# Performance work log

Measured on AMD Instinct MI355X. Metric: run time of the kernel, lower is better.

Reference implementation:

```python
import jax, jax.numpy as jnp
import numpy as np
from jax import lax

IMAGE_SIZE = 1280
STRIDE = 32
FMP = IMAGE_SIZE // STRIDE          # 40
BPC = 5                             # boxes per cell (5 anchors)
NUM_CLASSES = 80
NMS_THRESH = 0.5
CONF_THRESH = 0.3
N_BOX = FMP * FMP * BPC             # 8000 candidates
ANCHOR_SIZE = np.array([[17, 25], [55, 75], [92, 206], [202, 21], [289, 311]], dtype=np.float32)


def _make_anchors():
    # generate_anchors: per-cell (x,y) grid repeated for each of BPC anchors, tiled anchor wh
    ys, xs = jnp.meshgrid(jnp.arange(FMP, dtype=jnp.float32), jnp.arange(FMP, dtype=jnp.float32), indexing='ij')
    xy = jnp.stack([xs, ys], axis=-1).reshape(-1, 1, 2)                       # [HW,1,2]
    anchor_xy = jnp.broadcast_to(xy, (FMP * FMP, BPC, 2)).reshape(-1, 2)      # [N,2]
    anchor_wh = jnp.broadcast_to(jnp.asarray(ANCHOR_SIZE)[None], (FMP * FMP, BPC, 2)).reshape(-1, 2)
    return jnp.concatenate([anchor_xy, anchor_wh], axis=-1)                   # [N,4]


def setup_inputs() -> dict:
    key = jax.random.key(0)
    k = jax.random.split(key, 5)
    return {
        'cls_feat': jax.random.normal(k[0], (1, 512, FMP, FMP), jnp.float32),
        'reg_feat': jax.random.normal(k[1], (1, 512, FMP, FMP), jnp.float32),
        'w_obj': jax.random.normal(k[2], (BPC, 512), jnp.float32) * 0.02,
        'b_obj': jnp.zeros((BPC,), jnp.float32),
        'w_cls': jax.random.normal(k[3], (NUM_CLASSES * BPC, 512), jnp.float32) * 0.02,
        'b_cls': jnp.zeros((NUM_CLASSES * BPC,), jnp.float32),
        'w_reg': jax.random.normal(k[4], (4 * BPC, 512), jnp.float32) * 0.02,
        'b_reg': jnp.zeros((4 * BPC,), jnp.float32),
    }


def reference(cls_feat, reg_feat, w_obj, b_obj, w_cls, b_cls, w_reg, b_reg):
    # 1x1 convs as channel contractions, already permuted to NHWC like permute(0,2,3,1)
    obj = (jnp.einsum('bchw,oc->bhwo', reg_feat, w_obj) + b_obj).reshape(-1, 1)            # [N,1]
    cls = (jnp.einsum('bchw,oc->bhwo', cls_feat, w_cls) + b_cls).reshape(-1, NUM_CLASSES)  # [N,C]
    reg = (jnp.einsum('bchw,oc->bhwo', reg_feat, w_reg) + b_reg).reshape(-1, 4)            # [N,4]

    scores = jnp.sqrt(jax.nn.sigmoid(obj) * jax.nn.sigmoid(cls))                           # [N,C]

    # decode_boxes
    anchors = _make_anchors()
    ctr = (jax.nn.sigmoid(reg[:, :2]) + anchors[:, :2]) * STRIDE
    wh = jnp.exp(reg[:, 2:]) * anchors[:, 2:]
    bboxes = jnp.concatenate([ctr - wh * 0.5, ctr + wh * 0.5], axis=-1)                    # [N,4] x1y1x2y2

    # postprocess: per-box best class + confidence filter
    labels = jnp.argmax(scores, axis=1)
    score = jnp.take_along_axis(scores, labels[:, None], axis=1)[:, 0]
    valid = score >= CONF_THRESH

    # faithful to original nms(): it re-interprets decoded x1y1x2y2 as cxcywh before IoU
    b2 = jnp.concatenate([bboxes[:, :2] - bboxes[:, 2:] * 0.5,
                          bboxes[:, :2] + bboxes[:, 2:] * 0.5], axis=-1)

    # greedy per-class NMS == global greedy with cross-class IoU gated to 0
    order = jnp.argsort(-score)
    bs = b2[order]
    ls = labels[order]
    vs = valid[order]
    areas = (bs[:, 2] - bs[:, 0]) * (bs[:, 3] - bs[:, 1])
    xx1 = jnp.maximum(bs[:, None, 0], bs[None, :, 0])
    yy1 = jnp.maximum(bs[:, None, 1], bs[None, :, 1])
    xx2 = jnp.minimum(bs[:, None, 2], bs[None, :, 2])
    yy2 = jnp.minimum(bs[:, None, 3], bs[None, :, 3])
    inter = jnp.maximum(1e-10, xx2 - xx1) * jnp.maximum(1e-10, yy2 - yy1)
    iou = inter / (areas[:, None] + areas[None, :] - inter + 1e-14)                        # [N,N]
    same = ls[:, None] == ls[None, :]

    idx = jnp.arange(N_BOX)

    def body(k, supp):
        active = vs[k] & jnp.logical_not(supp[k])
        row = active & (iou[k] > NMS_THRESH) & same[k] & (idx > k)
        return supp | row

    supp = lax.fori_loop(0, N_BOX, body, jnp.zeros(N_BOX, bool))
    keep = jnp.zeros(N_BOX, bool).at[order].set(vs & jnp.logical_not(supp))

    # fixed-size masked outputs (original returns variable-length filtered arrays)
    return bboxes, score, labels, keep
```

## Files before the change

### kernel.cpp

```cpp
#include <hip/hip_runtime.h>
#include <math.h>

#define FMPX 40
#define NPOS 1600
#define NCLS 80
#define NBOX 8000
#define KDIM 512
#define CAP  256

__constant__ float c_aw[5] = {17.f, 55.f, 92.f, 202.f, 289.f};
__constant__ float c_ah[5] = {25.f, 75.f, 206.f, 21.f, 311.f};

__device__ __forceinline__ float sigf(float x) { return 1.0f / (1.0f + expf(-x)); }
__device__ __forceinline__ float rlanef(float v, int lane) {
    return __uint_as_float(__builtin_amdgcn_readlane(__float_as_uint(v), lane));
}

__global__ __launch_bounds__(64) void k_gemm(
    const float* __restrict__ cls_feat, const float* __restrict__ reg_feat,
    const float* __restrict__ w_obj, const float* __restrict__ b_obj,
    const float* __restrict__ w_cls, const float* __restrict__ b_cls,
    const float* __restrict__ w_reg, const float* __restrict__ b_reg,
    float* __restrict__ clsRaw,
    float* __restrict__ roRaw)
{
    __shared__ float Ws[4 * KDIM];
    const int mTile = blockIdx.x;
    const int nTile = blockIdx.y;
    const int hw0   = mTile * 128;
    const bool isCls = (nTile < 100);
    const float* feat = isCls ? cls_feat : reg_feat;
    const int lane = threadIdx.x;
    const int oBase = isCls ? nTile * 4 : (nTile - 100) * 4;

    for (int i = lane * 4; i < 4 * KDIM; i += 64 * 4) {
        int r = i >> 9, k = i & 511;
        const float* src;
        bool valid = true;
        if (isCls) {
            src = w_cls + (oBase + r) * KDIM + k;
        } else {
            int o = oBase + r;
            if (o < 5)       src = w_obj + o * KDIM + k;
            else if (o < 25) src = w_reg + (o - 5) * KDIM + k;
            else           { src = w_obj; valid = false; }
        }
        float4 v = valid ? *(const float4*)src : make_float4(0.f, 0.f, 0.f, 0.f);
        *(float4*)&Ws[i] = v;
    }

    float bias[4];
    bool ok[4];
#pragma unroll
    for (int j = 0; j < 4; j++) {
        int o = oBase + j;
        if (isCls)      { bias[j] = b_cls[o];     ok[j] = true; }
        else if (o < 5) { bias[j] = b_obj[o];     ok[j] = true; }
        else if (o < 25){ bias[j] = b_reg[o - 5]; ok[j] = true; }
        else            { bias[j] = 0.0f;         ok[j] = false; }
    }

    const bool ok1 = (hw0 + 64 + lane) < NPOS;
    const float* apa = feat + hw0 + lane;
    const float* apb = feat + (ok1 ? hw0 + 64 + lane : hw0 + lane);

    float A0a[8], A0b[8], A1a[8], A1b[8];
#pragma unroll
    for (int t = 0; t < 8; t++) { A0a[t] = apa[t * NPOS];       A0b[t] = apb[t * NPOS]; }
#pragma unroll
    for (int t = 0; t < 8; t++) { A1a[t] = apa[(8 + t) * NPOS]; A1b[t] = apb[(8 + t) * NPOS]; }

    __syncthreads();

    float acc[4], acd[4];
#pragma unroll
    for (int j = 0; j < 4; j++) { acc[j] = 0.f; acd[j] = 0.f; }

    for (int kk = 0; kk < KDIM - 16; kk += 16) {
#pragma unroll
        for (int j = 0; j < 4; j++) {
            const float* wp = &Ws[j * KDIM + kk];
#pragma unroll
            for (int t = 0; t < 8; t++) {
                acc[j] += A0a[t] * wp[t];
                acd[j] += A0b[t] * wp[t];
            }
        }
#pragma unroll
        for (int t = 0; t < 8; t++) { A0a[t] = apa[(kk + 16 + t) * NPOS]; A0b[t] = apb[(kk + 16 + t) * NPOS]; }
#pragma unroll
        for (int j = 0; j < 4; j++) {
            const float* wp = &Ws[j * KDIM + kk + 8];
#pragma unroll
            for (int t = 0; t < 8; t++) {
                acc[j] += A1a[t] * wp[t];
                acd[j] += A1b[t] * wp[t];
            }
        }
#pragma unroll
        for (int t = 0; t < 8; t++) { A1a[t] = apa[(kk + 24 + t) * NPOS]; A1b[t] = apb[(kk + 24 + t) * NPOS]; }
    }
    {
        const int kk = KDIM - 16;
#pragma unroll
        for (int j = 0; j < 4; j++) {
            const float* wp = &Ws[j * KDIM + kk];
#pragma unroll
            for (int t = 0; t < 8; t++) {
                acc[j] += A0a[t] * wp[t];
                acd[j] += A0b[t] * wp[t];
            }
        }
#pragma unroll
        for (int j = 0; j < 4; j++) {
            const float* wp = &Ws[j * KDIM + kk + 8];
#pragma unroll
            for (int t = 0; t < 8; t++) {
                acc[j] += A1a[t] * wp[t];
                acd[j] += A1b[t] * wp[t];
            }
        }
    }

    const int hw  = hw0 + lane;
    const int hw2 = hw + 64;
    if (isCls) {
        float4 r0 = make_float4(acc[0] + bias[0], acc[1] + bias[1],
                                acc[2] + bias[2], acc[3] + bias[3]);
        *(float4*)&clsRaw[hw * 400 + oBase] = r0;
        if (ok1) {
            float4 r1 = make_float4(acd[0] + bias[0], acd[1] + bias[1],
                                    acd[2] + bias[2], acd[3] + bias[3]);
            *(float4*)&clsRaw[hw2 * 400 + oBase] = r1;
        }
    } else {
#pragma unroll
        for (int j = 0; j < 4; j++) {
            int o = oBase + j;
            if (ok[j]) {
                roRaw[hw * 25 + o] = acc[j] + bias[j];
                if (ok1) roRaw[hw2 * 25 + o] = acd[j] + bias[j];
            }
        }
    }
}

__global__ __launch_bounds__(256) void k_box(
    const float* __restrict__ clsRaw, const float* __restrict__ roRaw,
    float* __restrict__ out,
    float4* __restrict__ nmsBox, float* __restrict__ nmsArea,
    float2* __restrict__ sl)
{
    const int n = blockIdx.x * 4 + (threadIdx.x >> 6);
    const int lane = threadIdx.x & 63;
    const int hw = n / 5, a = n % 5;

    const float sobj = sigf(roRaw[hw * 25 + a]);
    const float* cbase = clsRaw + hw * 400 + a * 80;

    const int l4 = (lane < 20) ? lane : 19;
    float4 cs = *(const float4*)(cbase + l4 * 4);

    float s0 = sqrtf(sobj * sigf(cs.x));
    float s1 = sqrtf(sobj * sigf(cs.y));
    float s2 = sqrtf(sobj * sigf(cs.z));
    float s3 = sqrtf(sobj * sigf(cs.w));
    float v = s0; int bi = l4 * 4;
    if (s1 > v) { v = s1; bi = l4 * 4 + 1; }
    if (s2 > v) { v = s2; bi = l4 * 4 + 2; }
    if (s3 > v) { v = s3; bi = l4 * 4 + 3; }
    if (lane >= 20) { v = -1.0f; bi = 0x7FFFFFFF; }

#pragma unroll
    for (int off = 32; off >= 1; off >>= 1) {
        float ov = __shfl_xor(v, off);
        int   oi = __shfl_xor(bi, off);
        if (ov > v || (ov == v && oi < bi)) { v = ov; bi = oi; }
    }

    if (lane == 0) {
        const float* rp = roRaw + hw * 25 + 5 + a * 4;
        float r0 = rp[0], r1 = rp[1], r2 = rp[2], r3 = rp[3];
        float gx = (float)(hw % FMPX), gy = (float)(hw / FMPX);
        float cx = (sigf(r0) + gx) * 32.0f;
        float cy = (sigf(r1) + gy) * 32.0f;
        float wv = expf(r2) * c_aw[a];
        float hv = expf(r3) * c_ah[a];
        float x1 = cx - wv * 0.5f, y1 = cy - hv * 0.5f;
        float x2 = cx + wv * 0.5f, y2 = cy + hv * 0.5f;

        out[n * 4 + 0] = x1; out[n * 4 + 1] = y1;
        out[n * 4 + 2] = x2; out[n * 4 + 3] = y2;
        out[32000 + n] = v;
        out[40000 + n] = (float)bi;
        out[48000 + n] = 0.0f;
        sl[n] = make_float2(v, (float)bi);

        float nx1 = x1 - x2 * 0.5f, ny1 = y1 - y2 * 0.5f;
        float nx2 = x1 + x2 * 0.5f, ny2 = y1 + y2 * 0.5f;
        nmsBox[n]  = make_float4(nx1, ny1, nx2, ny2);
        nmsArea[n] = (nx2 - nx1) * (ny2 - ny1);
    }
}

__global__ __launch_bounds__(64) void k_nms(
    const float2* __restrict__ sl,
    const float4* __restrict__ nmsBox, const float* __restrict__ nmsArea,
    float* __restrict__ keepOut)
{
    const int c = blockIdx.x;
    const int lane = threadIdx.x;

    __shared__ float ss[CAP];
    __shared__ int   si[CAP];
    __shared__ int   cnt;

    if (lane == 0) cnt = 0;
    __syncthreads();

    const float4* sl4 = (const float4*)sl;
    for (int base = 0; base < NBOX / 2; base += 512) {
        float4 buf[8];
#pragma unroll
        for (int b = 0; b < 8; b++) {
            int q = base + b * 64 + lane;
            buf[b] = (q < NBOX / 2) ? sl4[q] : make_float4(0.f, 0.f, 0.f, 0.f);
        }
#pragma unroll
        for (int b = 0; b < 8; b++) {
            int q = base + b * 64 + lane;
            if (q < NBOX / 2) {
                if (buf[b].x >= 0.3f && (int)buf[b].y == c) {
                    int t = atomicAdd(&cnt, 1);
                    if (t < CAP) { ss[t] = buf[b].x; si[t] = 2 * q; }
                }
                if (buf[b].z >= 0.3f && (int)buf[b].w == c) {
                    int t = atomicAdd(&cnt, 1);
                    if (t < CAP) { ss[t] = buf[b].z; si[t] = 2 * q + 1; }
                }
            }
        }
    }
    __syncthreads();

    int m = cnt;
    if (m > CAP) m = CAP;

    int P = 2;
    while (P < m) P <<= 1;
    for (int i = lane; i < P; i += 64) {
        if (i >= m) { ss[i] = -INFINITY; si[i] = 0x7FFFFFFF; }
    }
    __syncthreads();

    for (int size = 2; size <= P; size <<= 1) {
        for (int stride = size >> 1; stride > 0; stride >>= 1) {
            for (int t = lane; t < P / 2; t += 64) {
                int lo = 2 * stride * (t / stride) + (t % stride);
                int hi = lo + stride;
                bool desc = ((lo & size) == 0);
                float slo = ss[lo], shi = ss[hi];
                int   ilo = si[lo], ihi = si[hi];
                bool loBetter = (slo > shi) || (slo == shi && ilo < ihi);
                bool doSwap = desc ? !loBetter : loBetter;
                if (doSwap) { ss[lo] = shi; ss[hi] = slo; si[lo] = ihi; si[hi] = ilo; }
            }
            __syncthreads();
        }
    }

    float cx1[4], cy1[4], cx2[4], cy2[4], car[4];
    int   cidx[4];
    bool  cval[4];
#pragma unroll
    for (int s = 0; s < 4; s++) {
        int j = s * 64 + lane;
        cval[s] = (j < m);
        cidx[s] = 0;
        cx1[s] = 0.f; cy1[s] = 0.f; cx2[s] = 0.f; cy2[s] = 0.f; car[s] = 0.f;
        if (cval[s]) {
            int n = si[j];
            cidx[s] = n;
            float4 b = nmsBox[n];
            cx1[s] = b.x; cy1[s] = b.y; cx2[s] = b.z; cy2[s] = b.w;
            car[s] = nmsArea[n];
        }
    }

    int sp = 0;
#pragma unroll
    for (int s0 = 0; s0 < 4; s0++) {
        const int kend = (m < (s0 + 1) * 64) ? m : (s0 + 1) * 64;
        for (int k = s0 * 64; k < kend; k++) {
            const int owner = k & 63;
            int pk = __builtin_amdgcn_readlane(sp, owner);
            if ((pk >> s0) & 1) continue;

            float px1 = rlanef(cx1[s0], owner);
            float py1 = rlanef(cy1[s0], owner);
            float px2 = rlanef(cx2[s0], owner);
            float py2 = rlanef(cy2[s0], owner);
            float pa  = rlanef(car[s0], owner);

#pragma unroll
            for (int s = s0; s < 4; s++) {
                int j = s * 64 + lane;
                if (j > k && j < m) {
                    float xx1 = fmaxf(px1, cx1[s]);
                    float yy1 = fmaxf(py1, cy1[s]);
                    float xx2 = fminf(px2, cx2[s]);
                    float yy2 = fminf(py2, cy2[s]);
                    float inter = fmaxf(1e-10f, xx2 - xx1) * fmaxf(1e-10f, yy2 - yy1);
                    float iou = inter / ((pa + car[s] - inter) + 1e-14f);
                    if (iou > 0.5f) sp |= (1 << s);
                }
            }
        }
    }

#pragma unroll
    for (int s = 0; s < 4; s++) {
        if (cval[s] && !((sp >> s) & 1)) keepOut[cidx[s]] = 1.0f;
    }
}

extern "C" void kernel_launch(void* const* d_in, const int* in_sizes, int n_in,
                              void* d_out, int out_size, void* d_ws, size_t ws_size,
                              hipStream_t stream) {
    const float* cls_feat = (const float*)d_in[0];
    const float* reg_feat = (const float*)d_in[1];
    const float* w_obj    = (const float*)d_in[2];
    const float* b_obj    = (const float*)d_in[3];
    const float* w_cls    = (const float*)d_in[4];
    const float* b_cls    = (const float*)d_in[5];
    const float* w_reg    = (const float*)d_in[6];
    const float* b_reg    = (const float*)d_in[7];

    float* out = (float*)d_out;
    float* ws  = (float*)d_ws;

    float*  clsRaw    = ws;
    float*  roRaw     = ws + 640000;
    float4* nmsBox    = (float4*)(ws + 680000);
    float*  nmsArea   = ws + 712000;
    float2* sl        = (float2*)(ws + 720000);

    k_gemm<<<dim3(13, 107), 64, 0, stream>>>(cls_feat, reg_feat,
                                             w_obj, b_obj, w_cls, b_cls, w_reg, b_reg,
                                             clsRaw, roRaw);
    k_box<<<NBOX / 4, 256, 0, stream>>>(clsRaw, roRaw, out, nmsBox, nmsArea, sl);
    k_nms<<<NCLS, 64, 0, stream>>>(sl, nmsBox, nmsArea, out + 48000);
}
```

Before: 171.7 us.

## Deepen GEMM register prefetch and build per-class NMS candidate lists in box kernel

The GEMM kernel now keeps three 16-deep register buffers of feature loads in flight instead of two 8-deep ones, and issues them before the weight staging into shared memory. This is meant to hide more global-load latency. The box kernel now appends each candidate above threshold to a per-class list with a global atomic counter, which k_gemm zeroes. This removes the full 8000-entry scan each of the 80 NMS blocks used to do. The costs are more register pressure and global atomics, and the candidate order inside each list is nondeterministic, though it is sorted afterwards.

```diff
diff --git a/kernel.cpp b/kernel.cpp
--- a/kernel.cpp
+++ b/kernel.cpp
@@ -16,13 +16,37 @@
     return __uint_as_float(__builtin_amdgcn_readlane(__float_as_uint(v), lane));
 }
 
+__device__ __forceinline__ void loadA(float (&Ba)[16], float (&Bb)[16],
+                                      const float* __restrict__ apa,
+                                      const float* __restrict__ apb, int kbase) {
+#pragma unroll
+    for (int t = 0; t < 16; t++) {
+        Ba[t] = apa[(kbase + t) * NPOS];
+        Bb[t] = apb[(kbase + t) * NPOS];
+    }
+}
+__device__ __forceinline__ void consumeA(const float (&Ba)[16], const float (&Bb)[16],
+                                         const float* __restrict__ Ws, int kk,
+                                         float (&acc)[4], float (&acd)[4]) {
+#pragma unroll
+    for (int j = 0; j < 4; j++) {
+        const float* wp = &Ws[j * KDIM + kk];
+#pragma unroll
+        for (int t = 0; t < 16; t++) {
+            acc[j] += Ba[t] * wp[t];
+            acd[j] += Bb[t] * wp[t];
+        }
+    }
+}
+
 __global__ __launch_bounds__(64) void k_gemm(
     const float* __restrict__ cls_feat, const float* __restrict__ reg_feat,
     const float* __restrict__ w_obj, const float* __restrict__ b_obj,
     const float* __restrict__ w_cls, const float* __restrict__ b_cls,
     const float* __restrict__ w_reg, const float* __restrict__ b_reg,
     float* __restrict__ clsRaw,
-    float* __restrict__ roRaw)
+    float* __restrict__ roRaw,
+    int* __restrict__ counts)
 {
     __shared__ float Ws[4 * KDIM];
     const int mTile = blockIdx.x;
@@ -32,6 +56,20 @@
     const float* feat = isCls ? cls_feat : reg_feat;
     const int lane = threadIdx.x;
     const int oBase = isCls ? nTile * 4 : (nTile - 100) * 4;
+
+    if (mTile == 0 && nTile == 0) {
+        counts[lane] = 0;
+        if (lane < NCLS - 64) counts[64 + lane] = 0;
+    }
+
+    const bool ok1 = (hw0 + 64 + lane) < NPOS;
+    const float* apa = feat + hw0 + lane;
+    const float* apb = feat + (ok1 ? hw0 + 64 + lane : hw0 + lane);
+
+    float B0a[16], B0b[16], B1a[16], B1b[16], B2a[16], B2b[16];
+    loadA(B0a, B0b, apa, apb, 0);
+    loadA(B1a, B1b, apa, apb, 16);
+    loadA(B2a, B2b, apa, apb, 32);
 
     for (int i = lane * 4; i < 4 * KDIM; i += 64 * 4) {
         int r = i >> 9, k = i & 511;
@@ -60,67 +98,22 @@
         else            { bias[j] = 0.0f;         ok[j] = false; }
     }
 
-    const bool ok1 = (hw0 + 64 + lane) < NPOS;
-    const float* apa = feat + hw0 + lane;
-    const float* apb = feat + (ok1 ? hw0 + 64 + lane : hw0 + lane);
-
-    float A0a[8], A0b[8], A1a[8], A1b[8];
-#pragma unroll
-    for (int t = 0; t < 8; t++) { A0a[t] = apa[t * NPOS];       A0b[t] = apb[t * NPOS]; }
-#pragma unroll
-    for (int t = 0; t < 8; t++) { A1a[t] = apa[(8 + t) * NPOS]; A1b[t] = apb[(8 + t) * NPOS]; }
-
     __syncthreads();
 
-    float acc[4], acd[4];
-#pragma unroll
-    for (int j = 0; j < 4; j++) { acc[j] = 0.f; acd[j] = 0.f; }
-
-    for (int kk = 0; kk < KDIM - 16; kk += 16) {
-#pragma unroll
-        for (int j = 0; j < 4; j++) {
-            const float* wp = &Ws[j * KDIM + kk];
-#pragma unroll
-            for (int t = 0; t < 8; t++) {
-                acc[j] += A0a[t] * wp[t];
-                acd[j] += A0b[t] * wp[t];
-            }
-        }
-#pragma unroll
-        for (int t = 0; t < 8; t++) { A0a[t] = apa[(kk + 16 + t) * NPOS]; A0b[t] = apb[(kk + 16 + t) * NPOS]; }
-#pragma unroll
-        for (int j = 0; j < 4; j++) {
-            const float* wp = &Ws[j * KDIM + kk + 8];
-#pragma unroll
-            for (int t = 0; t < 8; t++) {
-                acc[j] += A1a[t] * wp[t];
-                acd[j] += A1b[t] * wp[t];
-            }
-        }
-#pragma unroll
-        for (int t = 0; t < 8; t++) { A1a[t] = apa[(kk + 24 + t) * NPOS]; A1b[t] = apb[(kk + 24 + t) * NPOS]; }
-    }
-    {
-        const int kk = KDIM - 16;
-#pragma unroll
-        for (int j = 0; j < 4; j++) {
-            const float* wp = &Ws[j * KDIM + kk];
-#pragma unroll
-            for (int t = 0; t < 8; t++) {
-                acc[j] += A0a[t] * wp[t];
-                acd[j] += A0b[t] * wp[t];
-            }
-        }
-#pragma unroll
-        for (int j = 0; j < 4; j++) {
-            const float* wp = &Ws[j * KDIM + kk + 8];
-#pragma unroll
-            for (int t = 0; t < 8; t++) {
-                acc[j] += A1a[t] * wp[t];
-                acd[j] += A1b[t] * wp[t];
-            }
-        }
-    }
+    float acc[4] = {0.f, 0.f, 0.f, 0.f};
+    float acd[4] = {0.f, 0.f, 0.f, 0.f};
+
+    int kk = 0;
+    for (; kk + 96 <= KDIM; kk += 48) {
+        consumeA(B0a, B0b, Ws, kk,      acc, acd);  loadA(B0a, B0b, apa, apb, kk + 48);
+        consumeA(B1a, B1b, Ws, kk + 16, acc, acd);  loadA(B1a, B1b, apa, apb, kk + 64);
+        consumeA(B2a, B2b, Ws, kk + 32, acc, acd);  loadA(B2a, B2b, apa, apb, kk + 80);
+    }
+    consumeA(B0a, B0b, Ws, 432, acc, acd);  loadA(B0a, B0b, apa, apb, 480);
+    consumeA(B1a, B1b, Ws, 448, acc, acd);  loadA(B1a, B1b, apa, apb, 496);
+    consumeA(B2a, B2b, Ws, 464, acc, acd);
+    consumeA(B0a, B0b, Ws, 480, acc, acd);
+    consumeA(B1a, B1b, Ws, 496, acc, acd);
 
     const int hw  = hw0 + lane;
     const int hw2 = hw + 64;
@@ -149,7 +142,7 @@
     const float* __restrict__ clsRaw, const float* __restrict__ roRaw,
     float* __restrict__ out,
     float4* __restrict__ nmsBox, float* __restrict__ nmsArea,
-    float2* __restrict__ sl)
+    float* __restrict__ listScore, int* __restrict__ listIdx, int* __restrict__ counts)
 {
     const int n = blockIdx.x * 4 + (threadIdx.x >> 6);
     const int lane = threadIdx.x & 63;
@@ -189,22 +182,26 @@
         float x1 = cx - wv * 0.5f, y1 = cy - hv * 0.5f;
         float x2 = cx + wv * 0.5f, y2 = cy + hv * 0.5f;
 
-        out[n * 4 + 0] = x1; out[n * 4 + 1] = y1;
-        out[n * 4 + 2] = x2; out[n * 4 + 3] = y2;
+        *(float4*)&out[n * 4] = make_float4(x1, y1, x2, y2);
         out[32000 + n] = v;
         out[40000 + n] = (float)bi;
         out[48000 + n] = 0.0f;
-        sl[n] = make_float2(v, (float)bi);
 
         float nx1 = x1 - x2 * 0.5f, ny1 = y1 - y2 * 0.5f;
         float nx2 = x1 + x2 * 0.5f, ny2 = y1 + y2 * 0.5f;
         nmsBox[n]  = make_float4(nx1, ny1, nx2, ny2);
         nmsArea[n] = (nx2 - nx1) * (ny2 - ny1);
+
+        if (v >= 0.3f) {
+            int p = atomicAdd(&counts[bi], 1);
+            if (p < CAP) { listScore[bi * CAP + p] = v; listIdx[bi * CAP + p] = n; }
+        }
     }
 }
 
 __global__ __launch_bounds__(64) void k_nms(
-    const float2* __restrict__ sl,
+    const float* __restrict__ listScore, const int* __restrict__ listIdx,
+    const int* __restrict__ counts,
     const float4* __restrict__ nmsBox, const float* __restrict__ nmsArea,
     float* __restrict__ keepOut)
 {
@@ -213,43 +210,15 @@
 
     __shared__ float ss[CAP];
     __shared__ int   si[CAP];
-    __shared__ int   cnt;
-
-    if (lane == 0) cnt = 0;
-    __syncthreads();
-
-    const float4* sl4 = (const float4*)sl;
-    for (int base = 0; base < NBOX / 2; base += 512) {
-        float4 buf[8];
-#pragma unroll
-        for (int b = 0; b < 8; b++) {
-            int q = base + b * 64 + lane;
-            buf[b] = (q < NBOX / 2) ? sl4[q] : make_float4(0.f, 0.f, 0.f, 0.f);
-        }
-#pragma unroll
-        for (int b = 0; b < 8; b++) {
-            int q = base + b * 64 + lane;
-            if (q < NBOX / 2) {
-                if (buf[b].x >= 0.3f && (int)buf[b].y == c) {
-                    int t = atomicAdd(&cnt, 1);
-                    if (t < CAP) { ss[t] = buf[b].x; si[t] = 2 * q; }
-                }
-                if (buf[b].z >= 0.3f && (int)buf[b].w == c) {
-                    int t = atomicAdd(&cnt, 1);
-                    if (t < CAP) { ss[t] = buf[b].z; si[t] = 2 * q + 1; }
-                }
-            }
-        }
-    }
-    __syncthreads();
-
-    int m = cnt;
+
+    int m = counts[c];
     if (m > CAP) m = CAP;
 
     int P = 2;
     while (P < m) P <<= 1;
     for (int i = lane; i < P; i += 64) {
-        if (i >= m) { ss[i] = -INFINITY; si[i] = 0x7FFFFFFF; }
+        if (i < m) { ss[i] = listScore[c * CAP + i]; si[i] = listIdx[c * CAP + i]; }
+        else       { ss[i] = -INFINITY;              si[i] = 0x7FFFFFFF; }
     }
     __syncthreads();
 
@@ -343,11 +312,15 @@
     float*  roRaw     = ws + 640000;
     float4* nmsBox    = (float4*)(ws + 680000);
     float*  nmsArea   = ws + 712000;
-    float2* sl        = (float2*)(ws + 720000);
+    float*  listScore = ws + 720000;
+    int*    listIdx   = (int*)(ws + 740480);
+    int*    counts    = (int*)(ws + 760960);
 
     k_gemm<<<dim3(13, 107), 64, 0, stream>>>(cls_feat, reg_feat,
                                              w_obj, b_obj, w_cls, b_cls, w_reg, b_reg,
-                                             clsRaw, roRaw);
-    k_box<<<NBOX / 4, 256, 0, stream>>>(clsRaw, roRaw, out, nmsBox, nmsArea, sl);
-    k_nms<<<NCLS, 64, 0, stream>>>(sl, nmsBox, nmsArea, out + 48000);
-}
+                                             clsRaw, roRaw, counts);
+    k_box<<<NBOX / 4, 256, 0, stream>>>(clsRaw, roRaw, out, nmsBox, nmsArea,
+                                        listScore, listIdx, counts);
+    k_nms<<<NCLS, 64, 0, stream>>>(listScore, listIdx, counts, nmsBox, nmsArea,
+                                   out + 48000);
+}
```

Measured after the change: 194.9 us. 1.13x slower.
